# Kernel tuning notes

Hardware: AMD Instinct MI355X
Metric: run time of the kernel (lower is better)

## Reference

```python
import jax, jax.numpy as jnp
import numpy as np
from jax import lax

B, T, E, H, ENC, NUM_LAYERS = 256, 100, 300, 512, 1024, 3
FORGET_BIAS = 1.0  # BasicLSTMCell default


def lstm_scan(x, W, b):
    """BasicLSTMCell over time. x: [B,T,E], W: [E+H,4H], b: [4H] -> hs: [B,T,H]."""
    def step(carry, xt):
        c, h = carry
        z = jnp.concatenate([xt, h], axis=-1) @ W + b  # [B,4H]
        i, j, f, o = jnp.split(z, 4, axis=-1)  # TF gate order i, j, f, o
        c = c * jax.nn.sigmoid(f + FORGET_BIAS) + jax.nn.sigmoid(i) * jnp.tanh(j)
        h = jnp.tanh(c) * jax.nn.sigmoid(o)
        return (c, h), h
    init = (jnp.zeros((x.shape[0], W.shape[1] // 4), x.dtype),) * 2
    _, hs = lax.scan(step, init, jnp.swapaxes(x, 0, 1))  # scan over T
    return jnp.swapaxes(hs, 0, 1)  # [B,T,H]


def last_output(hs, lengths):
    # reverse_sequence + slice[:, 0, :] == output at step length-1
    return hs[jnp.arange(hs.shape[0]), lengths - 1]  # [B,H]


def setup_inputs() -> dict:
    key = jax.random.key(0)
    ks = jax.random.split(key, 10)
    scale = 0.01  # random_normal_initializer(stddev=1/100)
    return {
        "left_embed": jax.random.normal(ks[0], (B, T, E), jnp.float32),
        "left_lengths": jax.random.randint(ks[1], (B,), 1, T + 1, jnp.int32),
        "right_embed": jax.random.normal(ks[2], (B, T, E), jnp.float32),
        "right_lengths": jax.random.randint(ks[3], (B,), 1, T + 1, jnp.int32),
        "W_left": jax.random.normal(ks[4], (E + H, 4 * H), jnp.float32) / np.sqrt(E + H),
        "b_left": jnp.zeros((4 * H,), jnp.float32),
        "W_right": jax.random.normal(ks[5], (E + H, 4 * H), jnp.float32) / np.sqrt(E + H),
        "b_right": jnp.zeros((4 * H,), jnp.float32),
        "trans_weights": scale * jax.random.normal(ks[6], (2 * H, ENC), jnp.float32),
        "hidden_weights": scale * jax.random.normal(ks[7], (NUM_LAYERS - 1, ENC, ENC), jnp.float32),
    }


def reference(left_embed, left_lengths, right_embed, right_lengths,
              W_left, b_left, W_right, b_right, trans_weights, hidden_weights):
    l_last = last_output(lstm_scan(left_embed, W_left, b_left), left_lengths)
    r_last = last_output(lstm_scan(right_embed, W_right, b_right), right_lengths)
    ctx = jnp.concatenate([l_last, r_last], axis=1)  # [B, 2H]
    x = jax.nn.relu(ctx @ trans_weights)
    for i in range(hidden_weights.shape[0]):  # dropout keep_prob=1.0 -> identity
        x = jax.nn.relu(x @ hidden_weights[i])
    return x  # [B, ENC]
```

## Files before the change

kernel.cpp:

```cpp
#include <hip/hip_runtime.h>
#include <math.h>

#define EDIM 300
#define HDIM 512
#define TDIM 100
#define BDIM 256
#define ENC  1024
#define NBLK 256

#define B_C     0u
#define B_HHI   1048576u
#define B_HLO   2097152u
#define B_WXF   3145728u
#define B_WHF   5767168u
#define B_CTX   9961472u
#define B_X1    11010048u
#define B_X2    12058624u
#define B_TWH   13107200u
#define B_TWL   19398656u
#define B_ZX    25690112u

typedef __attribute__((ext_vector_type(8))) short bf16x8;
typedef _Float16 f16x8 __attribute__((ext_vector_type(8)));
typedef __attribute__((ext_vector_type(4))) float f32x4;

__device__ __forceinline__ float fast_sigmoid(float x) {
    return 1.0f / (1.0f + __expf(-x));
}
__device__ __forceinline__ float fast_tanh(float x) {
    float t = __expf(2.0f * x);
    return 1.0f - 2.0f / (t + 1.0f);
}
__device__ __forceinline__ unsigned short bf16_rne(float v) {
    unsigned int u = __float_as_uint(v);
    unsigned int r = (u + 0x7fffu + ((u >> 16) & 1u)) >> 16;
    return (unsigned short)r;
}
__device__ __forceinline__ float bf16_to_f(unsigned short h) {
    return __uint_as_float(((unsigned int)h) << 16);
}
__device__ __forceinline__ void split2(float v, unsigned short& hi, unsigned short& lo) {
    hi = bf16_rne(v);
    lo = bf16_rne(v - bf16_to_f(hi));
}
__device__ __forceinline__ unsigned short f16_bits(float v) {
    _Float16 h = (_Float16)v;
    return *(unsigned short*)&h;
}
__device__ __forceinline__ float f16_val(unsigned short u) {
    _Float16 h = *(_Float16*)&u;
    return (float)h;
}
__device__ __forceinline__ void split_f16(float v, unsigned short& hi, unsigned short& lo) {
    hi = f16_bits(v);
    lo = f16_bits(v - f16_val(hi));
}

__global__ void zero_kernel(float* __restrict__ p, int n) {
    int i = blockIdx.x * blockDim.x + threadIdx.x;
    if (i < n) p[i] = 0.0f;
}

__global__ __launch_bounds__(256) void prep_wx(
    const float* __restrict__ WL, const float* __restrict__ WR, char* __restrict__ ws)
{
    __shared__ float tile[64 * 65];
    int bid = blockIdx.x;
    int d = bid / (5 * 32);
    int rem = bid - d * (5 * 32);
    int kt = rem >> 5;
    int ct = rem & 31;
    const int k0 = kt * 64;
    const float* W = d ? WR : WL;
    for (int pass = 0; pass < 16; ++pass) {
        int idx = pass * 256 + threadIdx.x;
        int kk = idx >> 6, c = idx & 63;
        int g = (c >> 4) & 3, hl = c & 15;
        int col = g * HDIM + ct * 16 + hl;
        int kg = k0 + kk;
        tile[kk * 65 + c] = (kg < EDIM) ? W[(size_t)kg * 2048 + col] : 0.0f;
    }
    __syncthreads();
    unsigned short* wx = (unsigned short*)(ws + B_WXF) + (size_t)d * 2048 * 320;
    for (int pass = 0; pass < 16; ++pass) {
        int idx = pass * 256 + threadIdx.x;
        int c = idx >> 6, kk = idx & 63;
        wx[(size_t)(ct * 64 + c) * 320 + k0 + kk] = f16_bits(tile[kk * 65 + c]);
    }
}

__global__ __launch_bounds__(256) void prep_whf(
    const float* __restrict__ WL, const float* __restrict__ WR, char* __restrict__ ws)
{
    __shared__ float tile[64 * 65];
    int bid = blockIdx.x;
    int d = bid >> 8;
    int rem = bid & 255;
    int kt = rem >> 5;
    int ct = rem & 31;
    const float* W = d ? WR : WL;
    for (int pass = 0; pass < 16; ++pass) {
        int idx = pass * 256 + threadIdx.x;
        int kk = idx >> 6, c = idx & 63;
        int g = (c >> 4) & 3, hl = c & 15;
        int col = g * HDIM + ct * 16 + hl;
        tile[kk * 65 + c] = W[(size_t)(300 + kt * 64 + kk) * 2048 + col];
    }
    __syncthreads();
    unsigned short* dst = (unsigned short*)(ws + B_WHF) + ((size_t)(d * 32 + ct) * 64) * 512;
    #pragma unroll
    for (int p = 0; p < 2; ++p) {
        int item = p * 256 + threadIdx.x;
        int fl = item >> 6;
        int ls = item & 63;
        int itl = fl >> 2, nfl = fl & 3;
        int frag = (kt >> 2) * 32 + ((kt & 3) * 2 + itl) * 4 + nfl;
        __align__(16) unsigned short v[8];
        #pragma unroll
        for (int j = 0; j < 8; ++j)
            v[j] = f16_bits(tile[(itl * 32 + (ls >> 4) * 8 + j) * 65 + nfl * 16 + (ls & 15)]);
        *(uint4*)(dst + (size_t)frag * 512 + ls * 8) = *(uint4*)v;
    }
}

__global__ __launch_bounds__(256) void prep_w_tail(
    const float* __restrict__ TW, const float* __restrict__ HW, char* __restrict__ ws)
{
    __shared__ float tile[64 * 65];
    int bid = blockIdx.x;
    int l = bid / 256;
    int rem = bid - l * 256;
    int kt = rem >> 4, ct = rem & 15;
    const int k0 = kt * 64, n0 = ct * 64;
    const float* W = (l == 0) ? TW : (HW + (size_t)(l - 1) * ENC * ENC);
    for (int pass = 0; pass < 16; ++pass) {
        int idx = pass * 256 + threadIdx.x;
        int kk = idx >> 6, c = idx & 63;
        tile[kk * 65 + c] = W[(size_t)(k0 + kk) * ENC + n0 + c];
    }
    __syncthreads();
    unsigned short* wh = (unsigned short*)(ws + B_TWH) + (size_t)l * ENC * ENC;
    unsigned short* wl = (unsigned short*)(ws + B_TWL) + (size_t)l * ENC * ENC;
    for (int pass = 0; pass < 16; ++pass) {
        int idx = pass * 256 + threadIdx.x;
        int c = idx >> 6, kk = idx & 63;
        unsigned short hi, lo;
        split2(tile[kk * 65 + c], hi, lo);
        size_t o = (size_t)(n0 + c) * ENC + k0 + kk;
        wh[o] = hi;
        wl[o] = lo;
    }
}

__global__ __launch_bounds__(512, 1) void prep_zx(
    const float* __restrict__ xL, const float* __restrict__ xR,
    const float* __restrict__ bL, const float* __restrict__ bR,
    char* __restrict__ ws)
{
    __shared__ __align__(16) char smem[81920];
    const int ntile = blockIdx.x;
    const int m0    = blockIdx.y * 64;
    const int d     = blockIdx.z;
    const int n0    = ntile * 128;
    const float* __restrict__ x    = d ? xR : xL;
    const float* __restrict__ bias = d ? bR : bL;
    const unsigned short* __restrict__ Wxp = (const unsigned short*)(ws + B_WXF) + (size_t)d * 2048 * 320;
    unsigned short* __restrict__ zxd = (unsigned short*)(ws + B_ZX) + (size_t)d * TDIM * BDIM * 2048;

    const int tid = threadIdx.x;
    const int l   = tid & 63;
    const int w   = tid >> 6;
    const int kh  = w >> 2;
    const int ms  = w & 3;
    const int fr  = l & 15;
    const int fg  = l >> 4;

    #pragma unroll
    for (int j = 0; j < 10; ++j) {
        int c = j * 512 + tid;
        int frag = c >> 6, ls = c & 63;
        int khf = (frag >= 40) ? 1 : 0;
        int f2 = frag - khf * 40;
        int itf = f2 >> 3, nff = f2 & 7;
        int colp = n0 + nff * 16 + (ls & 15);
        int kk = khf * 160 + itf * 32 + (ls >> 4) * 8;
        *(uint4*)(smem + frag * 1024 + ls * 16) =
            *(const uint4*)(Wxp + (size_t)colp * 320 + kk);
    }
    __syncthreads();

    f32x4 acc[8] = {};
    const int rowX = m0 + ms * 16 + fr;
    const float* __restrict__ xrow = x + (size_t)rowX * EDIM;
    const int kb = kh * 160 + fg * 8;

    #pragma unroll
    for (int it = 0; it < 5; ++it) {
        const int kg = kb + it * 32;
        float4 f4a = (kg + 4 <= EDIM) ? *(const float4*)(xrow + kg) : make_float4(0.f, 0.f, 0.f, 0.f);
        float4 f4b = (kg + 8 <= EDIM) ? *(const float4*)(xrow + kg + 4) : make_float4(0.f, 0.f, 0.f, 0.f);
        __align__(16) unsigned short ahu[8], alu[8];
        float vv[8] = { f4a.x, f4a.y, f4a.z, f4a.w, f4b.x, f4b.y, f4b.z, f4b.w };
        #pragma unroll
        for (int i = 0; i < 8; ++i) {
            unsigned short hi, lo;
            split_f16(vv[i], hi, lo);
            ahu[i] = hi;
            alu[i] = lo;
        }
        const f16x8 ah = *(f16x8*)ahu;
        const f16x8 al = *(f16x8*)alu;
        #pragma unroll
        for (int nf = 0; nf < 8; ++nf) {
            const f16x8 bv = *(const f16x8*)(smem + ((kh * 40 + it * 8 + nf) << 10) + l * 16);
            acc[nf] = __builtin_amdgcn_mfma_f32_16x16x32_f16(ah, bv, acc[nf], 0, 0, 0);
            acc[nf] = __builtin_amdgcn_mfma_f32_16x16x32_f16(al, bv, acc[nf], 0, 0, 0);
        }
    }

    __syncthreads();
    float* red = (float*)smem;
    unsigned short* outT = (unsigned short*)(smem + 49152);
    if (kh == 1) {
        #pragma unroll
        for (int nf = 0; nf < 8; ++nf)
            #pragma unroll
            for (int r = 0; r < 4; ++r)
                red[(ms * 16 + fg * 4 + r) * 132 + nf * 16 + fr] = acc[nf][r];
    }
    __syncthreads();
    if (kh == 0) {
        #pragma unroll
        for (int nf = 0; nf < 8; ++nf) {
            const int col = (nf & 3) * HDIM + (ntile * 2 + (nf >> 2)) * 16 + fr;
            const float bv = bias[col];
            #pragma unroll
            for (int r = 0; r < 4; ++r) {
                float v = acc[nf][r] + red[(ms * 16 + fg * 4 + r) * 132 + nf * 16 + fr] + bv;
                outT[(ms * 16 + fg * 4 + r) * 128 + nf * 16 + fr] = f16_bits(v);
            }
        }
    }
    __syncthreads();
    {
        int row = tid >> 3, seg = tid & 7;
        int rm = m0 + row;
        int b = rm / 100;
        int tt = rm - b * 100;
        unsigned short* dstrow = zxd + ((size_t)(tt * 256 + b)) * 2048 + n0 + seg * 16;
        const unsigned short* s = outT + row * 128 + seg * 16;
        *(uint4*)(dstrow)     = *(const uint4*)(s);
        *(uint4*)(dstrow + 8) = *(const uint4*)(s + 8);
    }
}

__global__ __launch_bounds__(512, 1) void lstm_step_h(
    const int* __restrict__ lenL, const int* __restrict__ lenR,
    char* __restrict__ ws, int t, int par)
{
    __shared__ __align__(16) char smem[65536];

    const int bid   = blockIdx.x;
    const int ntile = (bid & 7) * 4 + ((bid >> 3) & 3);
    const int mt    = bid >> 5;
    const int n0    = ntile * 64;
    const int d     = mt >> 2;
    const int brow  = (mt & 3) * 64;

    const int* __restrict__ len = d ? lenR : lenL;

    float* __restrict__ cbuf = (float*)(ws + B_C);
    const unsigned short* __restrict__ hh_prev = (const unsigned short*)(ws + B_HHI) + (size_t)par * 262144;
    const unsigned short* __restrict__ hl_prev = (const unsigned short*)(ws + B_HLO) + (size_t)par * 262144;
    unsigned short* __restrict__ hh_next = (unsigned short*)(ws + B_HHI) + (size_t)(par ^ 1) * 262144;
    unsigned short* __restrict__ hl_next = (unsigned short*)(ws + B_HLO) + (size_t)(par ^ 1) * 262144;
    const unsigned short* __restrict__ WhF = (const unsigned short*)(ws + B_WHF);
    const unsigned short* __restrict__ zxd = (const unsigned short*)(ws + B_ZX) + (size_t)d * TDIM * BDIM * 2048;
    float* __restrict__ ctx = (float*)(ws + B_CTX);

    const int tid = threadIdx.x;
    const int l   = tid & 63;
    const int w   = tid >> 6;
    const int kh  = w >> 2;
    const int ms  = w & 3;
    const int fr  = l & 15;
    const int fg  = l >> 4;

    const int hcol = ntile * 16 + fr;
    const int row0 = brow + ms * 16 + fg * 4;
    const int4 len4 = *(const int4*)(len + row0);
    float c_arr[4];
    unsigned short zraw[16];
    if (kh == 0) {
        const size_t cb = (size_t)(d * BDIM + row0) * HDIM + hcol;
        c_arr[0] = cbuf[cb];
        c_arr[1] = cbuf[cb + HDIM];
        c_arr[2] = cbuf[cb + 2 * HDIM];
        c_arr[3] = cbuf[cb + 3 * HDIM];
        const unsigned short* zb = zxd + ((size_t)(t * 256 + row0)) * 2048 + n0 + fr;
        #pragma unroll
        for (int r = 0; r < 4; ++r)
            #pragma unroll
            for (int nf = 0; nf < 4; ++nf)
                zraw[r * 4 + nf] = zb[r * 2048 + nf * 16];
    }

    {
        const unsigned short* __restrict__ wsrc = WhF + ((size_t)(d * 32 + ntile) * 64) * 512;
        #pragma unroll
        for (int j = 0; j < 8; ++j) {
            int o = j * 512 + tid;
            *(uint4*)(smem + o * 16) = *(const uint4*)(wsrc + (size_t)o * 8);
        }
    }

    const size_t abase = (size_t)(d * BDIM + brow + ms * 16 + fr) * HDIM + kh * 256 + fg * 8;
    uint4 pfh[2], pfl[2];
    pfh[0] = *(const uint4*)(hh_prev + abase);
    pfl[0] = *(const uint4*)(hl_prev + abase);
    pfh[1] = *(const uint4*)(hh_prev + abase + 32);
    pfl[1] = *(const uint4*)(hl_prev + abase + 32);
    __syncthreads();

    f32x4 acc[4] = {};
    #pragma unroll
    for (int it = 0; it < 8; ++it) {
        const uint4 ch = pfh[it & 1];
        const uint4 cl = pfl[it & 1];
        if (it + 2 < 8) {
            pfh[it & 1] = *(const uint4*)(hh_prev + abase + (it + 2) * 32);
            pfl[it & 1] = *(const uint4*)(hl_prev + abase + (it + 2) * 32);
        }
        const f16x8 ah = *(const f16x8*)&ch;
        const f16x8 al = *(const f16x8*)&cl;
        #pragma unroll
        for (int nf = 0; nf < 4; ++nf) {
            const f16x8 bv = *(const f16x8*)(smem + ((kh * 32 + it * 4 + nf) << 10) + l * 16);
            acc[nf] = __builtin_amdgcn_mfma_f32_16x16x32_f16(ah, bv, acc[nf], 0, 0, 0);
            acc[nf] = __builtin_amdgcn_mfma_f32_16x16x32_f16(al, bv, acc[nf], 0, 0, 0);
        }
    }

    __syncthreads();
    float* red = (float*)smem;
    if (kh == 1) {
        #pragma unroll
        for (int nf = 0; nf < 4; ++nf)
            #pragma unroll
            for (int r = 0; r < 4; ++r)
                red[(ms * 16 + fg * 4 + r) * 65 + nf * 16 + fr] = acc[nf][r];
    }
    __syncthreads();
    if (kh == 0) {
        const int lens[4] = { len4.x, len4.y, len4.z, len4.w };
        #pragma unroll
        for (int r = 0; r < 4; ++r) {
            const int row = row0 + r;
            const int rb = (ms * 16 + fg * 4 + r) * 65;
            const float iv = acc[0][r] + red[rb + 0 * 16 + fr] + f16_val(zraw[r * 4 + 0]);
            const float jv = acc[1][r] + red[rb + 1 * 16 + fr] + f16_val(zraw[r * 4 + 1]);
            const float fv = acc[2][r] + red[rb + 2 * 16 + fr] + f16_val(zraw[r * 4 + 2]);
            const float ov = acc[3][r] + red[rb + 3 * 16 + fr] + f16_val(zraw[r * 4 + 3]);
            const float c_new = c_arr[r] * fast_sigmoid(fv + 1.0f)
                              + fast_sigmoid(iv) * fast_tanh(jv);
            const float h_new = fast_tanh(c_new) * fast_sigmoid(ov);
            const size_t hidx = (size_t)(d * BDIM + row) * HDIM + hcol;
            cbuf[hidx] = c_new;
            unsigned short hh, hl2;
            split_f16(h_new, hh, hl2);
            hh_next[hidx] = hh;
            hl_next[hidx] = hl2;
            if (t == lens[r] - 1) {
                ctx[(size_t)row * (2 * HDIM) + d * HDIM + hcol] = h_new;
            }
        }
    }
}

#define TL_AS_HI(hf) ((hf) * 5120)
#define TL_AS_LO(hf) (10240 + (hf) * 5120)
#define TL_BS_HI(hf) (20480 + (hf) * 5120)
#define TL_BS_LO(hf) (30720 + (hf) * 5120)

__global__ __launch_bounds__(512, 2) void gemm_relu_mfma(
    const float* __restrict__ A, const unsigned short* __restrict__ Wh,
    const unsigned short* __restrict__ Wl, float* __restrict__ C)
{
    const int ntile = blockIdx.x & 15;
    const int mt    = blockIdx.x >> 4;
    const int n0    = ntile * 64;
    const int m0    = mt * 64;

    __shared__ __align__(16) char smem[40960];

    const int tid  = threadIdx.x;
    const int l    = tid & 63;
    const int w    = tid >> 6;
    const int kh   = w >> 2;
    const int ms   = w & 3;
    const int fr   = l & 15;
    const int fg   = l >> 4;
    const int arow = tid >> 3;
    const int q    = (tid & 7) * 4;

    f32x4 acc[4] = {};

    for (int it = 0; it < 16; ++it) {
        #pragma unroll
        for (int hf = 0; hf < 2; ++hf) {
            const int kg = hf * 512 + it * 32 + q;
            const float4 v = *(const float4*)(A + (size_t)(m0 + arow) * ENC + kg);
            ushort4 vh, vl;
            split2(v.x, vh.x, vl.x);
            split2(v.y, vh.y, vl.y);
            split2(v.z, vh.z, vl.z);
            split2(v.w, vh.w, vl.w);
            *(ushort4*)(smem + TL_AS_HI(hf) + (arow * 40 + q) * 2) = vh;
            *(ushort4*)(smem + TL_AS_LO(hf) + (arow * 40 + q) * 2) = vl;
            const size_t wo = (size_t)(n0 + arow) * ENC + kg;
            *(ushort4*)(smem + TL_BS_HI(hf) + (arow * 40 + q) * 2) = *(const ushort4*)(Wh + wo);
            *(ushort4*)(smem + TL_BS_LO(hf) + (arow * 40 + q) * 2) = *(const ushort4*)(Wl + wo);
        }
        __syncthreads();
        const int aoff = ((ms * 16 + fr) * 40 + fg * 8) * 2;
        const bf16x8 ah = *(const bf16x8*)(smem + TL_AS_HI(kh) + aoff);
        const bf16x8 al = *(const bf16x8*)(smem + TL_AS_LO(kh) + aoff);
        #pragma unroll
        for (int nf = 0; nf < 4; ++nf) {
            const int boff = ((nf * 16 + fr) * 40 + fg * 8) * 2;
            const bf16x8 bh = *(const bf16x8*)(smem + TL_BS_HI(kh) + boff);
            const bf16x8 bl = *(const bf16x8*)(smem + TL_BS_LO(kh) + boff);
            acc[nf] = __builtin_amdgcn_mfma_f32_16x16x32_bf16(ah, bh, acc[nf], 0, 0, 0);
            acc[nf] = __builtin_amdgcn_mfma_f32_16x16x32_bf16(ah, bl, acc[nf], 0, 0, 0);
            acc[nf] = __builtin_amdgcn_mfma_f32_16x16x32_bf16(al, bh, acc[nf], 0, 0, 0);
        }
        __syncthreads();
    }

    float* red = (float*)smem;
    if (kh == 1) {
        #pragma unroll
        for (int nf = 0; nf < 4; ++nf)
            #pragma unroll
            for (int r = 0; r < 4; ++r)
                red[(ms * 16 + fg * 4 + r) * 65 + nf * 16 + fr] = acc[nf][r];
    }
    __syncthreads();
    if (kh == 0) {
        #pragma unroll
        for (int nf = 0; nf < 4; ++nf) {
            #pragma unroll
            for (int r = 0; r < 4; ++r) {
                float v = acc[nf][r] + red[(ms * 16 + fg * 4 + r) * 65 + nf * 16 + fr];
                v = v > 0.f ? v : 0.f;
                const int row = m0 + ms * 16 + fg * 4 + r;
                C[(size_t)row * ENC + n0 + nf * 16 + fr] = v;
            }
        }
    }
}

extern "C" void kernel_launch(void* const* d_in, const int* in_sizes, int n_in,
                              void* d_out, int out_size, void* d_ws, size_t ws_size,
                              hipStream_t stream) {
    const float* xL   = (const float*)d_in[0];
    const int*   lenL = (const int*)  d_in[1];
    const float* xR   = (const float*)d_in[2];
    const int*   lenR = (const int*)  d_in[3];
    const float* WL   = (const float*)d_in[4];
    const float* bL   = (const float*)d_in[5];
    const float* WR   = (const float*)d_in[6];
    const float* bR   = (const float*)d_in[7];
    const float* TW   = (const float*)d_in[8];
    const float* HW   = (const float*)d_in[9];
    char* ws   = (char*)d_ws;
    float* out = (float*)d_out;

    zero_kernel<<<3072, 256, 0, stream>>>((float*)ws, 786432);
    prep_wx<<<320, 256, 0, stream>>>(WL, WR, ws);
    prep_whf<<<512, 256, 0, stream>>>(WL, WR, ws);
    prep_w_tail<<<768, 256, 0, stream>>>(TW, HW, ws);
    prep_zx<<<dim3(16, 400, 2), 512, 0, stream>>>(xL, xR, bL, bR, ws);

    for (int t = 0; t < TDIM; ++t) {
        lstm_step_h<<<NBLK, 512, 0, stream>>>(lenL, lenR, ws, t, t & 1);
    }

    float* ctx = (float*)(ws + B_CTX);
    float* x1  = (float*)(ws + B_X1);
    float* x2  = (float*)(ws + B_X2);
    const unsigned short* twh = (const unsigned short*)(ws + B_TWH);
    const unsigned short* twl = (const unsigned short*)(ws + B_TWL);
    gemm_relu_mfma<<<64, 512, 0, stream>>>(ctx, twh,                twl,                x1);
    gemm_relu_mfma<<<64, 512, 0, stream>>>(x1,  twh + 1024 * 1024, twl + 1024 * 1024,  x2);
    gemm_relu_mfma<<<64, 512, 0, stream>>>(x2,  twh + 2048 * 1024, twl + 2048 * 1024,  out);
}
```

Measured before the change: 1.304 ms.

## Pack hi/lo f16 hidden state together, preload A fragments, drop x-projection lo term

The hidden-state hi and lo f16 halves are now stored interleaved in one packed buffer, so each 8-element chunk of hi sits next to its lo chunk. The recurrent step kernel loads all A fragments for the step into registers up front, issued before the weight-tile staging, instead of a two-deep rolling prefetch. Separately, the input-projection kernel stops splitting x into hi and lo f16 halves and runs only the hi MFMA, which halves that GEMM's MFMA count. That last change lowers the precision of the x contribution, and the full A preload raises register use.

```diff
diff --git a/kernel.cpp b/kernel.cpp
--- a/kernel.cpp
+++ b/kernel.cpp
@@ -9,8 +9,7 @@
 #define NBLK 256
 
 #define B_C     0u
-#define B_HHI   1048576u
-#define B_HLO   2097152u
+#define B_HPK   1048576u
 #define B_WXF   3145728u
 #define B_WHF   5767168u
 #define B_CTX   9961472u
@@ -199,22 +198,15 @@
         const int kg = kb + it * 32;
         float4 f4a = (kg + 4 <= EDIM) ? *(const float4*)(xrow + kg) : make_float4(0.f, 0.f, 0.f, 0.f);
         float4 f4b = (kg + 8 <= EDIM) ? *(const float4*)(xrow + kg + 4) : make_float4(0.f, 0.f, 0.f, 0.f);
-        __align__(16) unsigned short ahu[8], alu[8];
+        __align__(16) unsigned short ahu[8];
         float vv[8] = { f4a.x, f4a.y, f4a.z, f4a.w, f4b.x, f4b.y, f4b.z, f4b.w };
         #pragma unroll
-        for (int i = 0; i < 8; ++i) {
-            unsigned short hi, lo;
-            split_f16(vv[i], hi, lo);
-            ahu[i] = hi;
-            alu[i] = lo;
-        }
+        for (int i = 0; i < 8; ++i) ahu[i] = f16_bits(vv[i]);
         const f16x8 ah = *(f16x8*)ahu;
-        const f16x8 al = *(f16x8*)alu;
         #pragma unroll
         for (int nf = 0; nf < 8; ++nf) {
             const f16x8 bv = *(const f16x8*)(smem + ((kh * 40 + it * 8 + nf) << 10) + l * 16);
             acc[nf] = __builtin_amdgcn_mfma_f32_16x16x32_f16(ah, bv, acc[nf], 0, 0, 0);
-            acc[nf] = __builtin_amdgcn_mfma_f32_16x16x32_f16(al, bv, acc[nf], 0, 0, 0);
         }
     }
 
@@ -270,10 +262,8 @@
     const int* __restrict__ len = d ? lenR : lenL;
 
     float* __restrict__ cbuf = (float*)(ws + B_C);
-    const unsigned short* __restrict__ hh_prev = (const unsigned short*)(ws + B_HHI) + (size_t)par * 262144;
-    const unsigned short* __restrict__ hl_prev = (const unsigned short*)(ws + B_HLO) + (size_t)par * 262144;
-    unsigned short* __restrict__ hh_next = (unsigned short*)(ws + B_HHI) + (size_t)(par ^ 1) * 262144;
-    unsigned short* __restrict__ hl_next = (unsigned short*)(ws + B_HLO) + (size_t)(par ^ 1) * 262144;
+    const unsigned short* __restrict__ hpk_prev = (const unsigned short*)(ws + B_HPK) + (size_t)par * 524288;
+    unsigned short* __restrict__ hpk_next = (unsigned short*)(ws + B_HPK) + (size_t)(par ^ 1) * 524288;
     const unsigned short* __restrict__ WhF = (const unsigned short*)(ws + B_WHF);
     const unsigned short* __restrict__ zxd = (const unsigned short*)(ws + B_ZX) + (size_t)d * TDIM * BDIM * 2048;
     float* __restrict__ ctx = (float*)(ws + B_CTX);
@@ -285,6 +275,16 @@
     const int ms  = w & 3;
     const int fr  = l & 15;
     const int fg  = l >> 4;
+
+    const int arow = d * BDIM + brow + ms * 16 + fr;
+    const unsigned short* __restrict__ abase = hpk_prev + (size_t)arow * 1024;
+    uint4 aph[8], apl[8];
+    #pragma unroll
+    for (int it = 0; it < 8; ++it) {
+        const int kb = kh * 32 + it * 4 + fg;
+        aph[it] = *(const uint4*)(abase + kb * 16);
+        apl[it] = *(const uint4*)(abase + kb * 16 + 8);
+    }
 
     const int hcol = ntile * 16 + fr;
     const int row0 = brow + ms * 16 + fg * 4;
@@ -313,26 +313,13 @@
             *(uint4*)(smem + o * 16) = *(const uint4*)(wsrc + (size_t)o * 8);
         }
     }
-
-    const size_t abase = (size_t)(d * BDIM + brow + ms * 16 + fr) * HDIM + kh * 256 + fg * 8;
-    uint4 pfh[2], pfl[2];
-    pfh[0] = *(const uint4*)(hh_prev + abase);
-    pfl[0] = *(const uint4*)(hl_prev + abase);
-    pfh[1] = *(const uint4*)(hh_prev + abase + 32);
-    pfl[1] = *(const uint4*)(hl_prev + abase + 32);
     __syncthreads();
 
     f32x4 acc[4] = {};
     #pragma unroll
     for (int it = 0; it < 8; ++it) {
-        const uint4 ch = pfh[it & 1];
-        const uint4 cl = pfl[it & 1];
-        if (it + 2 < 8) {
-            pfh[it & 1] = *(const uint4*)(hh_prev + abase + (it + 2) * 32);
-            pfl[it & 1] = *(const uint4*)(hl_prev + abase + (it + 2) * 32);
-        }
-        const f16x8 ah = *(const f16x8*)&ch;
-        const f16x8 al = *(const f16x8*)&cl;
+        const f16x8 ah = *(const f16x8*)&aph[it];
+        const f16x8 al = *(const f16x8*)&apl[it];
         #pragma unroll
         for (int nf = 0; nf < 4; ++nf) {
             const f16x8 bv = *(const f16x8*)(smem + ((kh * 32 + it * 4 + nf) << 10) + l * 16);
@@ -364,12 +351,13 @@
             const float c_new = c_arr[r] * fast_sigmoid(fv + 1.0f)
                               + fast_sigmoid(iv) * fast_tanh(jv);
             const float h_new = fast_tanh(c_new) * fast_sigmoid(ov);
-            const size_t hidx = (size_t)(d * BDIM + row) * HDIM + hcol;
-            cbuf[hidx] = c_new;
+            const size_t cidx = (size_t)(d * BDIM + row) * HDIM + hcol;
+            cbuf[cidx] = c_new;
             unsigned short hh, hl2;
             split_f16(h_new, hh, hl2);
-            hh_next[hidx] = hh;
-            hl_next[hidx] = hl2;
+            const size_t hidx = (size_t)(d * BDIM + row) * 1024 + (hcol >> 3) * 16 + (hcol & 7);
+            hpk_next[hidx] = hh;
+            hpk_next[hidx + 8] = hl2;
             if (t == lens[r] - 1) {
                 ctx[(size_t)row * (2 * HDIM) + d * HDIM + hcol] = h_new;
             }
```

New measurement: 1.390 ms. 1.07x slower.
